# Optimization experiments

Measured on AMD Instinct MI355X. Metric: run time of the kernel, lower is better.

The kernel has to match this reference:

```python
import jax, jax.numpy as jnp
import numpy as np
from jax import lax

B, C, O, H, W = 4, 64, 64, 128, 128
K, PAD = 3, 1


def conv3x3(x, w, b):
    # standard 3x3 conv, stride 1, pad 1, NCHW / OIHW
    y = lax.conv_general_dilated(x, w, window_strides=(1, 1),
                                 padding=((PAD, PAD), (PAD, PAD)))
    return y + b[None, :, None, None]


def deform_conv(x, offset, w, b):
    # torchvision DeformConv2d (v1, 1 offset group): offset is [B, 2*K*K, H, W]
    # with (dy, dx) interleaved per kernel tap; sample pos = p0 + p_k + offset.
    Bn, Cn, Hn, Wn = x.shape
    off = offset.reshape(Bn, K * K, 2, Hn, Wn)
    ky, kx = jnp.meshgrid(jnp.arange(K), jnp.arange(K), indexing='ij')
    ky = ky.reshape(-1).astype(x.dtype)  # [9]
    kx = kx.reshape(-1).astype(x.dtype)
    base_y = jnp.arange(Hn, dtype=x.dtype)[None, None, :, None] - PAD + ky[None, :, None, None]
    base_x = jnp.arange(Wn, dtype=x.dtype)[None, None, None, :] - PAD + kx[None, :, None, None]
    py = base_y + off[:, :, 0]  # [B,9,H,W]
    px = base_x + off[:, :, 1]
    y0 = jnp.floor(py)
    x0 = jnp.floor(px)
    ly = py - y0  # bilinear fractional weights
    lx = px - x0
    y0i = y0.astype(jnp.int32)
    x0i = x0.astype(jnp.int32)
    xflat = x.reshape(Bn, Cn, Hn * Wn)

    def gather(yi, xi):
        valid = ((yi >= 0) & (yi < Hn) & (xi >= 0) & (xi < Wn)).astype(x.dtype)
        idx = (jnp.clip(yi, 0, Hn - 1) * Wn + jnp.clip(xi, 0, Wn - 1)).reshape(Bn, 1, -1)
        v = jnp.take_along_axis(xflat, idx, axis=2).reshape(Bn, Cn, K * K, Hn, Wn)
        return v * valid[:, None]  # zero padding outside image

    v00 = gather(y0i, x0i)
    v01 = gather(y0i, x0i + 1)
    v10 = gather(y0i + 1, x0i)
    v11 = gather(y0i + 1, x0i + 1)
    wy = ly[:, None]  # [B,1,9,H,W]
    wx = lx[:, None]
    samp = (v00 * (1 - wy) * (1 - wx) + v01 * (1 - wy) * wx
            + v10 * wy * (1 - wx) + v11 * wy * wx)  # [B,C,9,H,W]
    out = jnp.einsum('bckhw,ock->bohw', samp, w.reshape(w.shape[0], Cn, K * K))
    return out + b[None, :, None, None]


def setup_inputs() -> dict:
    key = jax.random.key(0)
    ks = jax.random.split(key, 16)
    n = lambda k, s, sc: jax.random.normal(k, s, jnp.float32) * sc
    inp = {
        'ref': n(ks[0], (B, C, H, W), 1.0),
        'nbr': n(ks[1], (B, C, H, W), 1.0),
        # offset convs: small weights so predicted offsets stay O(1) pixels
        'w_off1': n(ks[2], (18, 2 * C, 3, 3), 0.01), 'b_off1': n(ks[3], (18,), 0.01),
        'w_d1': n(ks[4], (O, C, 3, 3), 0.05), 'b_d1': n(ks[5], (O,), 0.05),
        'w_off2': n(ks[6], (18, 2 * O, 3, 3), 0.01), 'b_off2': n(ks[7], (18,), 0.01),
        'w_d2': n(ks[8], (O, O, 3, 3), 0.05), 'b_d2': n(ks[9], (O,), 0.05),
        'w_off3': n(ks[10], (18, 2 * O, 3, 3), 0.01), 'b_off3': n(ks[11], (18,), 0.01),
        'w_d3': n(ks[12], (O, O, 3, 3), 0.05), 'b_d3': n(ks[13], (O,), 0.05),
    }
    return inp


def reference(ref, nbr, w_off1, b_off1, w_d1, b_d1, w_off2, b_off2, w_d2, b_d2,
              w_off3, b_off3, w_d3, b_d3):
    offset1 = conv3x3(jnp.concatenate([ref, nbr], axis=1), w_off1, b_off1)
    d1 = deform_conv(nbr, offset1, w_d1, b_d1)
    offset2 = conv3x3(jnp.concatenate([ref, d1], axis=1), w_off2, b_off2)
    d2 = deform_conv(d1, offset2, w_d2, b_d2)
    offset3 = conv3x3(jnp.concatenate([ref, d2], axis=1), w_off3, b_off3)
    d3 = deform_conv(d2, offset3, w_d3, b_d3)
    return d3
```

## Files before the change

kernel.cpp:

```cpp
#include <hip/hip_runtime.h>
#include <hip/hip_bf16.h>

#define BB 4
#define CC 64
#define HH 128
#define WW 128
#define HW (HH * WW)
#define TOTPIX (BB * HW)

typedef short bf16x8 __attribute__((ext_vector_type(8)));
typedef float f32x4 __attribute__((ext_vector_type(4)));

static __device__ __forceinline__ short f2bf(float f) {
  __hip_bfloat16 h = __float2bfloat16(f);
  return __builtin_bit_cast(short, h);
}
static __device__ __forceinline__ float bf2f(short s) {
  unsigned int u = ((unsigned int)(unsigned short)s) << 16;
  return __builtin_bit_cast(float, u);
}

static __device__ __forceinline__ void stage1k(const short* g, short* lds) {
  __builtin_amdgcn_global_load_lds(
      (const __attribute__((address_space(1))) unsigned int*)g,
      (__attribute__((address_space(3))) unsigned int*)lds, 16, 0, 0);
}

__global__ __launch_bounds__(256) void prep_all_kernel(
    const float* __restrict__ a, const float* __restrict__ b,
    short* __restrict__ oa, short* __restrict__ ob,
    const float* __restrict__ wd1, const float* __restrict__ wo1,
    short* __restrict__ wtd1, short* __restrict__ wtoff1,
    const float* __restrict__ wd2, const float* __restrict__ wo2,
    short* __restrict__ wtd2, short* __restrict__ wtoff2,
    const float* __restrict__ wd3, const float* __restrict__ wo3,
    short* __restrict__ wtd3, short* __restrict__ wtoff3) {
  __shared__ float tile[64][68];
  const int t = threadIdx.x;
  if (blockIdx.x < 1024) {
    const int bid = blockIdx.x;
    const int bb = bid >> 8;
    const int hw0 = (bid & 255) * 64;
    for (int s = 0; s < 2; s++) {
      const float* src = s ? b : a;
      short* dst = s ? ob : oa;
      if (s) __syncthreads();
      {
        const int lp = t & 15;
        for (int c = (t >> 4); c < 64; c += 16) {
          float4 v = *(const float4*)&src[((size_t)(bb * 64 + c)) * HW + hw0 + lp * 4];
          *(float4*)&tile[c][lp * 4] = v;
        }
      }
      __syncthreads();
      {
        const int px = t >> 2;
        const int seg = t & 3;
        bf16x8 s0, s1;
#pragma unroll
        for (int i = 0; i < 8; i++) s0[i] = f2bf(tile[seg * 16 + i][px]);
#pragma unroll
        for (int i = 0; i < 8; i++) s1[i] = f2bf(tile[seg * 16 + 8 + i][px]);
        short* dp = dst + ((size_t)(bid * 64 + px)) * 64 + seg * 16;
        *(bf16x8*)dp = s0;
        *(bf16x8*)(dp + 8) = s1;
      }
    }
  } else {
    const int pb = blockIdx.x - 1024;
    const int s = pb / 144;
    const float* wd = (s == 0) ? wd1 : (s == 1) ? wd2 : wd3;
    const float* wo = (s == 0) ? wo1 : (s == 1) ? wo2 : wo3;
    short* wtd = (s == 0) ? wtd1 : (s == 1) ? wtd2 : wtd3;
    short* wtoff = (s == 0) ? wtoff1 : (s == 1) ? wtoff2 : wtoff3;
    const int i = (pb % 144) * 256 + t;
    const int j = i & 7, l = (i >> 3) & 63, f = i >> 9;
    {
      int ot = f & 3, cf = (f >> 2) & 1, k = f >> 3;
      int o = ot * 16 + (l & 15), c = cf * 32 + (l >> 4) * 8 + j;
      wtd[i] = f2bf(wd[(o * 64 + c) * 9 + k]);
    }
    {
      int ot = f & 1, ks = f >> 1;
      int cs = ks & 3, k = ks >> 2;
      int o = ot * 16 + (l & 15), c = cs * 32 + (l >> 4) * 8 + j;
      wtoff[i] = (o < 18) ? f2bf(wo[(o * 128 + c) * 9 + k]) : (short)0;
    }
  }
}

__global__ __launch_bounds__(256, 4) void off_tile_kernel(
    const short* __restrict__ ref, const short* __restrict__ x2,
    const short* __restrict__ wtoff, const float* __restrict__ bias,
    float* __restrict__ out) {
  __shared__ short tile[2 * 6 * 24 * 64];
  int bid = blockIdx.x;
  bid = (bid & 7) * (gridDim.x >> 3) + (bid >> 3);
  const int tid = threadIdx.x;
  const int l = tid & 63;
  const int g = __builtin_amdgcn_readfirstlane(tid >> 6);
  const int col = l & 15, quad = l >> 4;
  const int b = bid >> 8;
  const int rem = bid & 255;
  const int h0 = (rem >> 3) * 4;
  const int w0 = (rem & 7) * 16;
  const int oy = h0 - 1, ox = w0 - 1;
  const int h = h0 + g, w = w0 + col;
  const int pix = ((b << 7) + h) * WW + w;

  const short* srcs[2] = {ref + (size_t)b * (HW * 64), x2 + (size_t)b * (HW * 64)};

  {
    const int tc = l >> 3;
    const int m = l & 7;
#pragma unroll
    for (int i = 0; i < 9; i++) {
      const int idx = g + i * 4;
      const int t = idx / 18;
      const int rr = (idx % 18) / 3, seg = idx % 3;
      const int iy = min(max(oy + rr, 0), HH - 1);
      const int tcol = seg * 8 + tc;
      const int ix = min(max(ox + tcol, 0), WW - 1);
      const int sc = (m - tcol) & 7;
      stage1k(srcs[t] + (((iy << 7) + ix) << 6) + sc * 8,
              &tile[((t * 6 + rr) * 24 + seg * 8) << 6]);
    }
  }

  f32x4 acc0 = {0.f, 0.f, 0.f, 0.f}, acc1 = {0.f, 0.f, 0.f, 0.f};
  const bf16x8* wp = (const bf16x8*)wtoff + l;

  __syncthreads();

#pragma unroll
  for (int k = 0; k < 9; k++) {
    const int ky = k / 3, kx = k - ky * 3;
    const int hh = h + ky - 1, ww2 = w + kx - 1;
    const bool valid = (hh >= 0) & (hh < HH) & (ww2 >= 0) & (ww2 < WW);
    const int tr = g + ky;
    const int tcx = col + kx;
#pragma unroll
    for (int cs = 0; cs < 4; cs++) {
      const int t = cs >> 1;
      const int chunk = (cs & 1) * 4 + quad;
      bf16x8 v = *(const bf16x8*)&tile[(((t * 6 + tr) * 24 + tcx) << 6) +
                                       (((chunk + tcx) & 7) << 3)];
      if (!valid) v = (bf16x8)(short)0;
      const int f = (k * 4 + cs) * 2;
      acc0 = __builtin_amdgcn_mfma_f32_16x16x32_bf16(wp[f * 64], v, acc0, 0, 0, 0);
      acc1 = __builtin_amdgcn_mfma_f32_16x16x32_bf16(wp[(f + 1) * 64], v, acc1, 0, 0, 0);
    }
  }

#pragma unroll
  for (int r = 0; r < 4; r++)
    out[(quad * 4 + r) * TOTPIX + pix] = acc0[r] + bias[quad * 4 + r];
  if (quad == 0) {
    out[16 * TOTPIX + pix] = acc1[0] + bias[16];
    out[17 * TOTPIX + pix] = acc1[1] + bias[17];
  }
}

#define TH 16
#define TWP 24
__global__ __launch_bounds__(512, 4) void deform_tile_kernel(
    const short* __restrict__ x, const float* __restrict__ off,
    const short* __restrict__ wtd, const float* __restrict__ bias,
    float* __restrict__ outf, short* __restrict__ outb) {
  __shared__ short tile[TH * TWP * 64];
  int bid = blockIdx.x;
  bid = (bid & 7) * (gridDim.x >> 3) + (bid >> 3);
  const int tid = threadIdx.x;
  const int l = tid & 63;
  const int wv = __builtin_amdgcn_readfirstlane(tid >> 6);
  const int col = l & 15, quad = l >> 4;
  const int b = bid >> 7;
  const int rem = bid & 127;
  const int h0 = (rem >> 3) * 8;
  const int w0 = (rem & 7) * 16;
  const int oy = h0 - 4, ox = w0 - 4;
  const int h = h0 + wv, w = w0 + col;
  const int pix = ((b << 7) + h) * WW + w;

  const short* xb = x + (size_t)b * (HW * 64);

  {
    const int tc = ((l >> 3) & 7);
    const int m = l & 7;
#pragma unroll
    for (int i = 0; i < 6; i++) {
      const int idx = wv + i * 8;
      const int r = idx / 3, seg = idx % 3;
      const int iy = min(max(oy + r, 0), HH - 1);
      const int tcol = seg * 8 + tc;
      const int ix = min(max(ox + tcol, 0), WW - 1);
      const int sc = (m - tcol) & 7;
      stage1k(xb + (((iy << 7) + ix) << 6) + sc * 8,
              &tile[((r * TWP + seg * 8) << 6)]);
    }
  }

  float offv[18];
#pragma unroll
  for (int j = 0; j < 18; j++) offv[j] = off[j * TOTPIX + pix];

  f32x4 acc[4];
#pragma unroll
  for (int ot = 0; ot < 4; ot++)
#pragma unroll
    for (int r = 0; r < 4; r++) acc[ot][r] = 0.f;

  const int c0g = quad * 8;
  const bf16x8* wp = (const bf16x8*)wtd + l;

  __syncthreads();

#pragma unroll
  for (int k = 0; k < 9; k++) {
    const int ky = k / 3, kx = k - ky * 3;
    const float py = (float)(h - 1 + ky) + offv[2 * k];
    const float pxx = (float)(w - 1 + kx) + offv[2 * k + 1];
    const float y0f = floorf(py), x0f = floorf(pxx);
    const float ly = py - y0f, lx = pxx - x0f;
    const int y0 = (int)y0f, x0 = (int)x0f;
    const int y1 = y0 + 1, x1 = x0 + 1;
    float w00 = (1.f - ly) * (1.f - lx), w01 = (1.f - ly) * lx;
    float w10 = ly * (1.f - lx), w11 = ly * lx;
    if (y0 < 0 || y0 >= HH) { w00 = 0.f; w01 = 0.f; }
    if (y1 < 0 || y1 >= HH) { w10 = 0.f; w11 = 0.f; }
    if (x0 < 0 || x0 >= WW) { w00 = 0.f; w10 = 0.f; }
    if (x1 < 0 || x1 >= WW) { w01 = 0.f; w11 = 0.f; }
    const int cy0 = min(max(y0, 0), HH - 1), cy1 = min(max(y1, 0), HH - 1);
    const int cx0 = min(max(x0, 0), WW - 1), cx1 = min(max(x1, 0), WW - 1);

    const int ty0 = cy0 - oy, ty1 = cy1 - oy;
    const int tx0 = cx0 - ox, tx1 = cx1 - ox;
    const bool intile = (ty0 >= 0) & (ty1 < TH) & (tx0 >= 0) & (tx1 < TWP);

    bf16x8 v00a, v00b, v01a, v01b, v10a, v10b, v11a, v11b;
    if (__builtin_amdgcn_ballot_w64(intile) == ~0ull) {
      const int p00 = ((ty0 * TWP + tx0) << 6);
      const int p01 = ((ty0 * TWP + tx1) << 6);
      const int p10 = ((ty1 * TWP + tx0) << 6);
      const int p11 = ((ty1 * TWP + tx1) << 6);
      v00a = *(const bf16x8*)&tile[p00 + (((quad + tx0) & 7) << 3)];
      v00b = *(const bf16x8*)&tile[p00 + (((quad + 4 + tx0) & 7) << 3)];
      v01a = *(const bf16x8*)&tile[p01 + (((quad + tx1) & 7) << 3)];
      v01b = *(const bf16x8*)&tile[p01 + (((quad + 4 + tx1) & 7) << 3)];
      v10a = *(const bf16x8*)&tile[p10 + (((quad + tx0) & 7) << 3)];
      v10b = *(const bf16x8*)&tile[p10 + (((quad + 4 + tx0) & 7) << 3)];
      v11a = *(const bf16x8*)&tile[p11 + (((quad + tx1) & 7) << 3)];
      v11b = *(const bf16x8*)&tile[p11 + (((quad + 4 + tx1) & 7) << 3)];
    } else {
      const int p00 = ((cy0 * WW + cx0) << 6) + c0g;
      const int p01 = ((cy0 * WW + cx1) << 6) + c0g;
      const int p10 = ((cy1 * WW + cx0) << 6) + c0g;
      const int p11 = ((cy1 * WW + cx1) << 6) + c0g;
      v00a = *(const bf16x8*)(xb + p00);
      v00b = *(const bf16x8*)(xb + p00 + 32);
      v01a = *(const bf16x8*)(xb + p01);
      v01b = *(const bf16x8*)(xb + p01 + 32);
      v10a = *(const bf16x8*)(xb + p10);
      v10b = *(const bf16x8*)(xb + p10 + 32);
      v11a = *(const bf16x8*)(xb + p11);
      v11b = *(const bf16x8*)(xb + p11 + 32);
    }

    bf16x8 bs0, bs1;
#pragma unroll
    for (int j = 0; j < 8; j++) {
      float sa = bf2f(v00a[j]) * w00 + bf2f(v01a[j]) * w01 +
                 bf2f(v10a[j]) * w10 + bf2f(v11a[j]) * w11;
      bs0[j] = f2bf(sa);
      float sb = bf2f(v00b[j]) * w00 + bf2f(v01b[j]) * w01 +
                 bf2f(v10b[j]) * w10 + bf2f(v11b[j]) * w11;
      bs1[j] = f2bf(sb);
    }

    acc[0] = __builtin_amdgcn_mfma_f32_16x16x32_bf16(wp[(k * 8 + 0) * 64], bs0, acc[0], 0, 0, 0);
    acc[1] = __builtin_amdgcn_mfma_f32_16x16x32_bf16(wp[(k * 8 + 1) * 64], bs0, acc[1], 0, 0, 0);
    acc[2] = __builtin_amdgcn_mfma_f32_16x16x32_bf16(wp[(k * 8 + 2) * 64], bs0, acc[2], 0, 0, 0);
    acc[3] = __builtin_amdgcn_mfma_f32_16x16x32_bf16(wp[(k * 8 + 3) * 64], bs0, acc[3], 0, 0, 0);
    acc[0] = __builtin_amdgcn_mfma_f32_16x16x32_bf16(wp[(k * 8 + 4) * 64], bs1, acc[0], 0, 0, 0);
    acc[1] = __builtin_amdgcn_mfma_f32_16x16x32_bf16(wp[(k * 8 + 5) * 64], bs1, acc[1], 0, 0, 0);
    acc[2] = __builtin_amdgcn_mfma_f32_16x16x32_bf16(wp[(k * 8 + 6) * 64], bs1, acc[2], 0, 0, 0);
    acc[3] = __builtin_amdgcn_mfma_f32_16x16x32_bf16(wp[(k * 8 + 7) * 64], bs1, acc[3], 0, 0, 0);
  }

#pragma unroll
  for (int ot = 0; ot < 4; ot++)
#pragma unroll
    for (int r = 0; r < 4; r++)
      acc[ot][r] += bias[ot * 16 + quad * 4 + r];

  if (outb) {
#pragma unroll
    for (int ot = 0; ot < 4; ot++) {
      short4 sv;
      sv.x = f2bf(acc[ot][0]); sv.y = f2bf(acc[ot][1]);
      sv.z = f2bf(acc[ot][2]); sv.w = f2bf(acc[ot][3]);
      *(short4*)(outb + (size_t)pix * 64 + ot * 16 + quad * 4) = sv;
    }
  }
  if (outf) {
    const int hw = pix & (HW - 1);
#pragma unroll
    for (int ot = 0; ot < 4; ot++)
#pragma unroll
      for (int r = 0; r < 4; r++) {
        const int o = ot * 16 + quad * 4 + r;
        outf[(size_t)b * (CC * HW) + (size_t)o * HW + hw] = acc[ot][r];
      }
  }
}

extern "C" void kernel_launch(void* const* d_in, const int* in_sizes, int n_in,
                              void* d_out, int out_size, void* d_ws, size_t ws_size,
                              hipStream_t stream) {
  const float* ref    = (const float*)d_in[0];
  const float* nbr    = (const float*)d_in[1];
  const float* w_off1 = (const float*)d_in[2];
  const float* b_off1 = (const float*)d_in[3];
  const float* w_d1   = (const float*)d_in[4];
  const float* b_d1   = (const float*)d_in[5];
  const float* w_off2 = (const float*)d_in[6];
  const float* b_off2 = (const float*)d_in[7];
  const float* w_d2   = (const float*)d_in[8];
  const float* b_d2   = (const float*)d_in[9];
  const float* w_off3 = (const float*)d_in[10];
  const float* b_off3 = (const float*)d_in[11];
  const float* w_d3   = (const float*)d_in[12];
  const float* b_d3   = (const float*)d_in[13];

  float* out = (float*)d_out;
  char* ws = (char*)d_ws;
  float* off_buf = (float*)(ws);
  short* ref_bf  = (short*)(ws + 5242880);
  short* nbr_bf  = (short*)(ws + 13631488);
  short* d1_bf   = (short*)(ws + 22020096);
  short* d2_bf   = (short*)(ws + 30408704);
  short* wtd1    = (short*)(ws + 38797312);
  short* wtd2    = (short*)(ws + 38871040);
  short* wtd3    = (short*)(ws + 38944768);
  short* wtoff1  = (short*)(ws + 39018496);
  short* wtoff2  = (short*)(ws + 39092224);
  short* wtoff3  = (short*)(ws + 39165952);

  prep_all_kernel<<<1456, 256, 0, stream>>>(
      ref, nbr, ref_bf, nbr_bf,
      w_d1, w_off1, wtd1, wtoff1,
      w_d2, w_off2, wtd2, wtoff2,
      w_d3, w_off3, wtd3, wtoff3);

  const int nblk_oc = BB * HW / 64;
  const int nblk_df = BB * HW / 128;

  off_tile_kernel<<<nblk_oc, 256, 0, stream>>>(ref_bf, nbr_bf, wtoff1, b_off1, off_buf);
  deform_tile_kernel<<<nblk_df, 512, 0, stream>>>(nbr_bf, off_buf, wtd1, b_d1, nullptr, d1_bf);
  off_tile_kernel<<<nblk_oc, 256, 0, stream>>>(ref_bf, d1_bf, wtoff2, b_off2, off_buf);
  deform_tile_kernel<<<nblk_df, 512, 0, stream>>>(d1_bf, off_buf, wtd2, b_d2, nullptr, d2_bf);
  off_tile_kernel<<<nblk_oc, 256, 0, stream>>>(ref_bf, d2_bf, wtoff3, b_off3, off_buf);
  deform_tile_kernel<<<nblk_df, 512, 0, stream>>>(d2_bf, off_buf, wtd3, b_d3, out, nullptr);
}
```

Before: 118.6 us.

## Fuse offset conv into deformable conv kernel per stage

Merges the offset-prediction 3x3 conv into the deformable-conv kernel. Each block now stages a ref tile alongside the x tile in LDS, computes the 18 offsets with MFMA, and passes them through LDS instead of a global fp32 offset buffer. This removes three kernel launches and the global write and reload of the offset tensor. In exchange LDS use per block goes up, launch bounds drop to 2 blocks per CU, and two extra barriers are added.

Measured after the change: 111.1 us. -6.3%, faster.

```diff
diff --git a/kernel.cpp b/kernel.cpp
--- a/kernel.cpp
+++ b/kernel.cpp
@@ -89,85 +89,16 @@
   }
 }
 
-__global__ __launch_bounds__(256, 4) void off_tile_kernel(
-    const short* __restrict__ ref, const short* __restrict__ x2,
-    const short* __restrict__ wtoff, const float* __restrict__ bias,
-    float* __restrict__ out) {
-  __shared__ short tile[2 * 6 * 24 * 64];
-  int bid = blockIdx.x;
-  bid = (bid & 7) * (gridDim.x >> 3) + (bid >> 3);
-  const int tid = threadIdx.x;
-  const int l = tid & 63;
-  const int g = __builtin_amdgcn_readfirstlane(tid >> 6);
-  const int col = l & 15, quad = l >> 4;
-  const int b = bid >> 8;
-  const int rem = bid & 255;
-  const int h0 = (rem >> 3) * 4;
-  const int w0 = (rem & 7) * 16;
-  const int oy = h0 - 1, ox = w0 - 1;
-  const int h = h0 + g, w = w0 + col;
-  const int pix = ((b << 7) + h) * WW + w;
-
-  const short* srcs[2] = {ref + (size_t)b * (HW * 64), x2 + (size_t)b * (HW * 64)};
-
-  {
-    const int tc = l >> 3;
-    const int m = l & 7;
-#pragma unroll
-    for (int i = 0; i < 9; i++) {
-      const int idx = g + i * 4;
-      const int t = idx / 18;
-      const int rr = (idx % 18) / 3, seg = idx % 3;
-      const int iy = min(max(oy + rr, 0), HH - 1);
-      const int tcol = seg * 8 + tc;
-      const int ix = min(max(ox + tcol, 0), WW - 1);
-      const int sc = (m - tcol) & 7;
-      stage1k(srcs[t] + (((iy << 7) + ix) << 6) + sc * 8,
-              &tile[((t * 6 + rr) * 24 + seg * 8) << 6]);
-    }
-  }
-
-  f32x4 acc0 = {0.f, 0.f, 0.f, 0.f}, acc1 = {0.f, 0.f, 0.f, 0.f};
-  const bf16x8* wp = (const bf16x8*)wtoff + l;
-
-  __syncthreads();
-
-#pragma unroll
-  for (int k = 0; k < 9; k++) {
-    const int ky = k / 3, kx = k - ky * 3;
-    const int hh = h + ky - 1, ww2 = w + kx - 1;
-    const bool valid = (hh >= 0) & (hh < HH) & (ww2 >= 0) & (ww2 < WW);
-    const int tr = g + ky;
-    const int tcx = col + kx;
-#pragma unroll
-    for (int cs = 0; cs < 4; cs++) {
-      const int t = cs >> 1;
-      const int chunk = (cs & 1) * 4 + quad;
-      bf16x8 v = *(const bf16x8*)&tile[(((t * 6 + tr) * 24 + tcx) << 6) +
-                                       (((chunk + tcx) & 7) << 3)];
-      if (!valid) v = (bf16x8)(short)0;
-      const int f = (k * 4 + cs) * 2;
-      acc0 = __builtin_amdgcn_mfma_f32_16x16x32_bf16(wp[f * 64], v, acc0, 0, 0, 0);
-      acc1 = __builtin_amdgcn_mfma_f32_16x16x32_bf16(wp[(f + 1) * 64], v, acc1, 0, 0, 0);
-    }
-  }
-
-#pragma unroll
-  for (int r = 0; r < 4; r++)
-    out[(quad * 4 + r) * TOTPIX + pix] = acc0[r] + bias[quad * 4 + r];
-  if (quad == 0) {
-    out[16 * TOTPIX + pix] = acc1[0] + bias[16];
-    out[17 * TOTPIX + pix] = acc1[1] + bias[17];
-  }
-}
-
 #define TH 16
 #define TWP 24
-__global__ __launch_bounds__(512, 4) void deform_tile_kernel(
-    const short* __restrict__ x, const float* __restrict__ off,
+#define RTH 10
+__global__ __launch_bounds__(512, 2) void fused_stage_kernel(
+    const short* __restrict__ ref, const short* __restrict__ x,
+    const short* __restrict__ wtoff, const float* __restrict__ boff,
     const short* __restrict__ wtd, const float* __restrict__ bias,
     float* __restrict__ outf, short* __restrict__ outb) {
-  __shared__ short tile[TH * TWP * 64];
+  __shared__ short xt[TH * TWP * 64];
+  __shared__ short rt[RTH * TWP * 64];
   int bid = blockIdx.x;
   bid = (bid & 7) * (gridDim.x >> 3) + (bid >> 3);
   const int tid = threadIdx.x;
@@ -183,6 +114,7 @@
   const int pix = ((b << 7) + h) * WW + w;
 
   const short* xb = x + (size_t)b * (HW * 64);
+  const short* rb = ref + (size_t)b * (HW * 64);
 
   {
     const int tc = ((l >> 3) & 7);
@@ -196,13 +128,70 @@
       const int ix = min(max(ox + tcol, 0), WW - 1);
       const int sc = (m - tcol) & 7;
       stage1k(xb + (((iy << 7) + ix) << 6) + sc * 8,
-              &tile[((r * TWP + seg * 8) << 6)]);
-    }
-  }
+              &xt[((r * TWP + seg * 8) << 6)]);
+    }
+#pragma unroll
+    for (int i = 0; i < 4; i++) {
+      const int idx = wv + i * 8;
+      if (idx < 30) {
+        const int r = idx / 3, seg = idx % 3;
+        const int iy = min(max(h0 - 1 + r, 0), HH - 1);
+        const int tcol = seg * 8 + tc;
+        const int ix = min(max(ox + tcol, 0), WW - 1);
+        const int sc = (m - tcol) & 7;
+        stage1k(rb + (((iy << 7) + ix) << 6) + sc * 8,
+                &rt[((r * TWP + seg * 8) << 6)]);
+      }
+    }
+  }
+
+  __syncthreads();
+
+  f32x4 oacc0 = {0.f, 0.f, 0.f, 0.f}, oacc1 = {0.f, 0.f, 0.f, 0.f};
+  {
+    const bf16x8* wpo = (const bf16x8*)wtoff + l;
+#pragma unroll
+    for (int k = 0; k < 9; k++) {
+      const int ky = k / 3, kx = k - ky * 3;
+      const int hh = h + ky - 1, ww2 = w + kx - 1;
+      const bool valid = (hh >= 0) & (hh < HH) & (ww2 >= 0) & (ww2 < WW);
+      const int trr = wv + ky;
+      const int trx = wv + ky + 3;
+      const int tcx = col + kx + 3;
+#pragma unroll
+      for (int cs = 0; cs < 4; cs++) {
+        const int chunk = (cs & 1) * 4 + quad;
+        const int sw = ((chunk + tcx) & 7) << 3;
+        bf16x8 v;
+        if (cs < 2)
+          v = *(const bf16x8*)&rt[((trr * TWP + tcx) << 6) + sw];
+        else
+          v = *(const bf16x8*)&xt[((trx * TWP + tcx) << 6) + sw];
+        if (!valid) v = (bf16x8)(short)0;
+        const int f = (k * 4 + cs) * 2;
+        oacc0 = __builtin_amdgcn_mfma_f32_16x16x32_bf16(wpo[f * 64], v, oacc0, 0, 0, 0);
+        oacc1 = __builtin_amdgcn_mfma_f32_16x16x32_bf16(wpo[(f + 1) * 64], v, oacc1, 0, 0, 0);
+      }
+    }
+  }
+
+  __syncthreads();
+
+  float* offlds = (float*)rt;
+  {
+    float* po = offlds + (wv * 16 + col) * 20;
+#pragma unroll
+    for (int r = 0; r < 4; r++) po[quad * 4 + r] = oacc0[r] + boff[quad * 4 + r];
+    if (quad == 0) {
+      po[16] = oacc1[0] + boff[16];
+      po[17] = oacc1[1] + boff[17];
+    }
+  }
+  __syncthreads();
 
   float offv[18];
 #pragma unroll
-  for (int j = 0; j < 18; j++) offv[j] = off[j * TOTPIX + pix];
+  for (int j = 0; j < 18; j++) offv[j] = offlds[(wv * 16 + col) * 20 + j];
 
   f32x4 acc[4];
 #pragma unroll
@@ -212,8 +201,6 @@
 
   const int c0g = quad * 8;
   const bf16x8* wp = (const bf16x8*)wtd + l;
-
-  __syncthreads();
 
 #pragma unroll
   for (int k = 0; k < 9; k++) {
@@ -243,14 +230,14 @@
       const int p01 = ((ty0 * TWP + tx1) << 6);
       const int p10 = ((ty1 * TWP + tx0) << 6);
       const int p11 = ((ty1 * TWP + tx1) << 6);
-      v00a = *(const bf16x8*)&tile[p00 + (((quad + tx0) & 7) << 3)];
-      v00b = *(const bf16x8*)&tile[p00 + (((quad + 4 + tx0) & 7) << 3)];
-      v01a = *(const bf16x8*)&tile[p01 + (((quad + tx1) & 7) << 3)];
-      v01b = *(const bf16x8*)&tile[p01 + (((quad + 4 + tx1) & 7) << 3)];
-      v10a = *(const bf16x8*)&tile[p10 + (((quad + tx0) & 7) << 3)];
-      v10b = *(const bf16x8*)&tile[p10 + (((quad + 4 + tx0) & 7) << 3)];
-      v11a = *(const bf16x8*)&tile[p11 + (((quad + tx1) & 7) << 3)];
-      v11b = *(const bf16x8*)&tile[p11 + (((quad + 4 + tx1) & 7) << 3)];
+      v00a = *(const bf16x8*)&xt[p00 + (((quad + tx0) & 7) << 3)];
+      v00b = *(const bf16x8*)&xt[p00 + (((quad + 4 + tx0) & 7) << 3)];
+      v01a = *(const bf16x8*)&xt[p01 + (((quad + tx1) & 7) << 3)];
+      v01b = *(const bf16x8*)&xt[p01 + (((quad + 4 + tx1) & 7) << 3)];
+      v10a = *(const bf16x8*)&xt[p10 + (((quad + tx0) & 7) << 3)];
+      v10b = *(const bf16x8*)&xt[p10 + (((quad + 4 + tx0) & 7) << 3)];
+      v11a = *(const bf16x8*)&xt[p11 + (((quad + tx1) & 7) << 3)];
+      v11b = *(const bf16x8*)&xt[p11 + (((quad + 4 + tx1) & 7) << 3)];
     } else {
       const int p00 = ((cy0 * WW + cx0) << 6) + c0g;
       const int p01 = ((cy0 * WW + cx1) << 6) + c0g;
@@ -334,7 +321,6 @@
 
   float* out = (float*)d_out;
   char* ws = (char*)d_ws;
-  float* off_buf = (float*)(ws);
   short* ref_bf  = (short*)(ws + 5242880);
   short* nbr_bf  = (short*)(ws + 13631488);
   short* d1_bf   = (short*)(ws + 22020096);
@@ -352,13 +338,12 @@
       w_d2, w_off2, wtd2, wtoff2,
       w_d3, w_off3, wtd3, wtoff3);
 
-  const int nblk_oc = BB * HW / 64;
-  const int nblk_df = BB * HW / 128;
-
-  off_tile_kernel<<<nblk_oc, 256, 0, stream>>>(ref_bf, nbr_bf, wtoff1, b_off1, off_buf);
-  deform_tile_kernel<<<nblk_df, 512, 0, stream>>>(nbr_bf, off_buf, wtd1, b_d1, nullptr, d1_bf);
-  off_tile_kernel<<<nblk_oc, 256, 0, stream>>>(ref_bf, d1_bf, wtoff2, b_off2, off_buf);
-  deform_tile_kernel<<<nblk_df, 512, 0, stream>>>(d1_bf, off_buf, wtd2, b_d2, nullptr, d2_bf);
-  off_tile_kernel<<<nblk_oc, 256, 0, stream>>>(ref_bf, d2_bf, wtoff3, b_off3, off_buf);
-  deform_tile_kernel<<<nblk_df, 512, 0, stream>>>(d2_bf, off_buf, wtd3, b_d3, out, nullptr);
-}
+  const int nblk = BB * HW / 128;
+
+  fused_stage_kernel<<<nblk, 512, 0, stream>>>(
+      ref_bf, nbr_bf, wtoff1, b_off1, wtd1, b_d1, nullptr, d1_bf);
+  fused_stage_kernel<<<nblk, 512, 0, stream>>>(
+      ref_bf, d1_bf, wtoff2, b_off2, wtd2, b_d2, nullptr, d2_bf);
+  fused_stage_kernel<<<nblk, 512, 0, stream>>>(
+      ref_bf, d2_bf, wtoff3, b_off3, wtd3, b_d3, out, nullptr);
+}
```
